# Performance work log

Hardware: AMD Instinct MI355X
Metric: run time of the kernel (lower is better)

## Reference

```python
import jax, jax.numpy as jnp
import numpy as np

HIDDEN = 4096
N_HEADS = 32
HEAD_DIM = HIDDEN // N_HEADS
BATCH = 2
SEQ = 2048
ROPE_BASE = 10000.0


def _rope_cos_sin(seq_len, head_dim, dtype):
    inv_freq = 1.0 / (ROPE_BASE ** (jnp.arange(0, head_dim, 2, dtype=jnp.float32) / head_dim))
    t = jnp.arange(seq_len, dtype=jnp.float32)
    freqs = t[:, None] * inv_freq[None, :]          # (seq, head_dim/2)
    emb = jnp.concatenate([freqs, freqs], axis=-1)  # (seq, head_dim)
    return jnp.cos(emb).astype(dtype), jnp.sin(emb).astype(dtype)


def _rotate_half(x):
    d = x.shape[-1] // 2
    return jnp.concatenate([-x[..., d:], x[..., :d]], axis=-1)


def setup_inputs() -> dict:
    key = jax.random.key(0)
    ks = jax.random.split(key, 5)
    s = 1.0 / np.sqrt(HIDDEN)
    return {
        "hidden_states": jax.random.normal(ks[0], (BATCH, SEQ, HIDDEN), dtype=jnp.float32),
        "Wq": jax.random.normal(ks[1], (HIDDEN, HIDDEN), dtype=jnp.float32) * s,
        "Wk": jax.random.normal(ks[2], (HIDDEN, HIDDEN), dtype=jnp.float32) * s,
        "Wv": jax.random.normal(ks[3], (HIDDEN, HIDDEN), dtype=jnp.float32) * s,
        "Wo": jax.random.normal(ks[4], (HIDDEN, HIDDEN), dtype=jnp.float32) * s,
    }


def reference(hidden_states, Wq, Wk, Wv, Wo):
    b, s, _ = hidden_states.shape
    # nn.Linear: y = x @ W.T
    q = hidden_states @ Wq.T
    k = hidden_states @ Wk.T
    v = hidden_states @ Wv.T
    # (b, s, h, d) -> (b, h, s, d)
    q = q.reshape(b, s, N_HEADS, HEAD_DIM).transpose(0, 2, 1, 3)
    k = k.reshape(b, s, N_HEADS, HEAD_DIM).transpose(0, 2, 1, 3)
    v = v.reshape(b, s, N_HEADS, HEAD_DIM).transpose(0, 2, 1, 3)
    cos, sin = _rope_cos_sin(s, HEAD_DIM, hidden_states.dtype)  # (s, d)
    cos = cos[None, None]  # (1,1,s,d)
    sin = sin[None, None]
    q = q * cos + _rotate_half(q) * sin
    k = k * cos + _rotate_half(k) * sin
    scores = jnp.einsum("bhqd,bhkd->bhqk", q, k) / np.sqrt(HEAD_DIM).astype(np.float32)
    attn = jax.nn.softmax(scores, axis=-1)
    out = jnp.einsum("bhqk,bhkd->bhqd", attn, v)
    out = out.transpose(0, 2, 1, 3).reshape(b, s, HIDDEN)
    return out @ Wo.T
```

## Files before the change

kernel.cpp:

```cpp
#include <hip/hip_runtime.h>
#include <hip/hip_bf16.h>

typedef unsigned int u32;

typedef __attribute__((ext_vector_type(4)))  float f32x4;
typedef __attribute__((ext_vector_type(16))) float f32x16;
typedef __attribute__((ext_vector_type(8)))  short s16x8;
typedef __attribute__((ext_vector_type(4)))  short s16x4;
typedef __attribute__((ext_vector_type(2)))  short s16x2;

#define MFMA16(acc, a, b) asm("v_mfma_f32_16x16x32_bf16 %0, %1, %2, %0" : "+v"(acc) : "v"(a), "v"(b))
#define MFMA32(acc, a, b) asm("v_mfma_f32_32x32x16_bf16 %0, %1, %2, %0" : "+v"(acc) : "v"(a), "v"(b))

__device__ __forceinline__ short f2bf(float f) {
  u32 u = __float_as_uint(f);
  return (short)((u + 0x7fffu + ((u >> 16) & 1u)) >> 16);
}
__device__ __forceinline__ float bf2f(short h) {
  return __uint_as_float(((u32)(unsigned short)h) << 16);
}
__device__ __forceinline__ void gload_lds16(const void* g, void* l) {
  __builtin_amdgcn_global_load_lds((const __attribute__((address_space(1))) u32*)g,
                                   (__attribute__((address_space(3))) u32*)l, 16, 0, 0);
}

__global__ __launch_bounds__(256) void cvt_f32_bf16(const float* __restrict__ in,
                                                    short* __restrict__ out, int n8) {
  int i = blockIdx.x * 256 + threadIdx.x;
  if (i >= n8) return;
  const f32x4* p = (const f32x4*)in;
  f32x4 a = p[2 * i], b = p[2 * i + 1];
  s16x8 o;
#pragma unroll
  for (int j = 0; j < 4; ++j) { o[j] = f2bf(a[j]); o[4 + j] = f2bf(b[j]); }
  *(s16x8*)(out + 8 * (size_t)i) = o;
}

__global__ __launch_bounds__(256) void rope_tables(float* __restrict__ ct, float* __restrict__ st) {
  int tid = blockIdx.x * 256 + threadIdx.x;
  int i = tid & 63, s = tid >> 6;
  float inv = exp2f(-(float)(2 * i) * (13.287712379549449f / 128.0f));
  float ang = (float)s * inv;
  ct[tid] = cosf(ang);
  st[tid] = sinf(ang);
}

__global__ __launch_bounds__(256) void rope_apply(short* __restrict__ x, const float* __restrict__ ct,
                                                  const float* __restrict__ st, float scale) {
  int tid = blockIdx.x * 256 + threadIdx.x;
  int quad = tid & 15;
  int h = (tid >> 4) & 31;
  int s = (tid >> 9) & 2047;
  int b = tid >> 20;
  size_t off = ((size_t)(b * 2048 + s)) * 4096 + h * 128 + quad * 4;
  s16x4 lo = *(s16x4*)(x + off);
  s16x4 hi = *(s16x4*)(x + off + 64);
  f32x4 c = *(const f32x4*)(ct + s * 64 + quad * 4);
  f32x4 sn = *(const f32x4*)(st + s * 64 + quad * 4);
  s16x4 nlo, nhi;
#pragma unroll
  for (int j = 0; j < 4; ++j) {
    float fl = bf2f(lo[j]), fh = bf2f(hi[j]);
    nlo[j] = f2bf((fl * c[j] - fh * sn[j]) * scale);
    nhi[j] = f2bf((fh * c[j] + fl * sn[j]) * scale);
  }
  *(s16x4*)(x + off) = nlo;
  *(s16x4*)(x + off + 64) = nhi;
}

template <int MODE>
__global__ __launch_bounds__(512) void gemm_nt(const short* __restrict__ A, const short* __restrict__ B,
                                               void* __restrict__ Cv, int M, int N, int K) {
  __shared__ short lds[65536];
  const int tid = threadIdx.x, lane = tid & 63, wid = tid >> 6;
  const int nbn = N >> 8;
  const int nwg = (M >> 8) * nbn;
  int bid = blockIdx.x;
  bid = (bid & 7) * (nwg >> 3) + (bid >> 3);
  const int m0 = (bid / nbn) << 8, n0 = (bid % nbn) << 8;
  const int wm = wid >> 2, wn = wid & 3;
  const int l15 = lane & 15, l16 = lane >> 4;
  const int r8 = lane >> 3, c8 = lane & 7;
  const int sw8 = (c8 ^ r8) << 3;

  f32x4 acc[8][4] = {};
  const int nt = K >> 6;

#pragma unroll
  for (int c = 0; c < 4; ++c) {
    const int chunk = wid * 4 + c;
    const int row = chunk * 8 + r8;
    gload_lds16(A + (size_t)(m0 + row) * K + sw8, &lds[chunk * 512]);
    gload_lds16(B + (size_t)(n0 + row) * K + sw8, &lds[32768 + chunk * 512]);
  }
  __syncthreads();

  for (int t = 0; t < nt; ++t) {
    const int bb = (t & 1) << 14;
    const int nb = bb ^ 16384;
    const short* As = &lds[bb];
    const short* Bs = &lds[32768 + bb];
    if (t + 1 < nt) {
      const int kt2 = (t + 1) << 6;
#pragma unroll
      for (int c = 0; c < 4; ++c) {
        const int chunk = wid * 4 + c;
        const int row = chunk * 8 + r8;
        gload_lds16(A + (size_t)(m0 + row) * K + kt2 + sw8, &lds[nb + chunk * 512]);
        gload_lds16(B + (size_t)(n0 + row) * K + kt2 + sw8, &lds[32768 + nb + chunk * 512]);
      }
    }
#pragma unroll
    for (int ph = 0; ph < 4; ++ph) {
      const int mh = ph >> 1, kc = ph & 1;
      s16x8 af[4], bfr[4];
#pragma unroll
      for (int i = 0; i < 4; ++i) {
        const int ra = wm * 128 + mh * 64 + i * 16 + l15;
        const int rb = wn * 64 + i * 16 + l15;
        const int cb = kc * 64 + l16 * 16;
        af[i]  = *(const s16x8*)((const char*)As + ra * 128 + (cb ^ ((ra & 7) << 4)));
        bfr[i] = *(const s16x8*)((const char*)Bs + rb * 128 + (cb ^ ((rb & 7) << 4)));
      }
#pragma unroll
      for (int i = 0; i < 4; ++i)
#pragma unroll
        for (int j = 0; j < 4; ++j) MFMA16(acc[mh * 4 + i][j], af[i], bfr[j]);
    }
    __syncthreads();
  }

  float* Cf = (float*)Cv;
  short* Cs = (short*)Cv;
  const int mrb = m0 + wm * 128 + l16 * 4;
  const int ncb = n0 + wn * 64 + l15;
#pragma unroll
  for (int mi = 0; mi < 8; ++mi)
#pragma unroll
    for (int ni = 0; ni < 4; ++ni)
#pragma unroll
      for (int r = 0; r < 4; ++r) {
        const int mm = mrb + mi * 16 + r;
        const int nn = ncb + ni * 16;
        const float v = acc[mi][ni][r];
        if constexpr (MODE == 0) {
          Cf[(size_t)mm * N + nn] = v;
        } else if constexpr (MODE == 1) {
          Cs[(size_t)mm * N + nn] = f2bf(v);
        } else {
          size_t idx = ((size_t)((mm >> 11) * 32 + (nn >> 7)) * 128 + (nn & 127)) * 2048 + (mm & 2047);
          Cs[idx] = f2bf(v);
        }
      }
}

__global__ __launch_bounds__(256) void attn_fwd(const short* __restrict__ Q, const short* __restrict__ K,
                                                const short* __restrict__ V, short* __restrict__ O) {
  __shared__ short Klds[64 * 136];
  __shared__ short Vt[128 * 72];
  __shared__ short Plds[4 * 32 * 72];
  const int tid = threadIdx.x, lane = tid & 63, wid = tid >> 6;
  const int q31 = lane & 31, hh = lane >> 5;
  int bid = blockIdx.x;
  bid = (bid & 7) * 128 + (bid >> 3);
  const int bh = bid >> 4, qt = bid & 15;
  const int b = bh >> 5, h = bh & 31;
  const size_t base = (size_t)b * 2048 * 4096 + h * 128;
  const short* Vg = V + ((size_t)(b * 32 + h)) * 128 * 2048;
  const int q0 = qt * 128 + wid * 32;

  s16x8 qf[8];
#pragma unroll
  for (int kc = 0; kc < 8; ++kc)
    qf[kc] = *(const s16x8*)(Q + base + (size_t)(q0 + q31) * 4096 + kc * 16 + hh * 8);

  f32x16 o[4] = {};
  float lsum = 0.0f;
  const float L2E = 1.44269504f, BIAS = 14.4269504f;

  for (int kv0 = 0; kv0 < 2048; kv0 += 64) {
    __syncthreads();
#pragma unroll
    for (int j = 0; j < 4; ++j) {
      int ci = tid + j * 256;
      int row = ci >> 4, cc = ci & 15;
      *(s16x8*)(&Klds[row * 136 + cc * 8]) =
          *(const s16x8*)(K + base + (size_t)(kv0 + row) * 4096 + cc * 8);
    }
#pragma unroll
    for (int j = 0; j < 4; ++j) {
      int ci = tid + j * 256;
      int row = ci >> 3, cc = ci & 7;
      *(s16x8*)(&Vt[row * 72 + cc * 8]) =
          *(const s16x8*)(Vg + (size_t)row * 2048 + kv0 + cc * 8);
    }
    __syncthreads();

    f32x16 st[2] = {};
    __builtin_amdgcn_s_setprio(1);
#pragma unroll
    for (int t = 0; t < 2; ++t)
#pragma unroll
      for (int kc = 0; kc < 8; ++kc) {
        s16x8 ak = *(const s16x8*)(&Klds[(t * 32 + q31) * 136 + kc * 16 + hh * 8]);
        MFMA32(st[t], ak, qf[kc]);
      }
    __builtin_amdgcn_s_setprio(0);

    float rs = 0.0f;
#pragma unroll
    for (int t = 0; t < 2; ++t)
#pragma unroll
      for (int r = 0; r < 16; ++r) {
        float p = exp2f(__builtin_fmaf(st[t][r], L2E, -BIAS));
        st[t][r] = p;
        rs += p;
      }
    rs += __shfl_xor(rs, 32);
    lsum += rs;

    short* Pw = &Plds[wid * 2304 + q31 * 72];
#pragma unroll
    for (int t = 0; t < 2; ++t)
#pragma unroll
      for (int rr = 0; rr < 16; rr += 2) {
        int kv = t * 32 + (rr & 3) + 8 * (rr >> 2) + 4 * hh;
        s16x2 pk;
        pk[0] = f2bf(st[t][rr]);
        pk[1] = f2bf(st[t][rr + 1]);
        *(s16x2*)(Pw + kv) = pk;
      }

    __builtin_amdgcn_s_setprio(1);
#pragma unroll
    for (int kc = 0; kc < 4; ++kc) {
      s16x8 bp = *(const s16x8*)(Pw + kc * 16 + hh * 8);
#pragma unroll
      for (int dt = 0; dt < 4; ++dt) {
        s16x8 av = *(const s16x8*)(&Vt[(dt * 32 + q31) * 72 + kc * 16 + hh * 8]);
        MFMA32(o[dt], av, bp);
      }
    }
    __builtin_amdgcn_s_setprio(0);
  }

  const float invl = 1.0f / lsum;
  short* Og = O + base + (size_t)(q0 + q31) * 4096;
#pragma unroll
  for (int dt = 0; dt < 4; ++dt)
#pragma unroll
    for (int g = 0; g < 4; ++g) {
      s16x4 w;
#pragma unroll
      for (int j = 0; j < 4; ++j) w[j] = f2bf(o[dt][g * 4 + j] * invl);
      *(s16x4*)(Og + dt * 32 + g * 8 + 4 * hh) = w;
    }
}

extern "C" void kernel_launch(void* const* d_in, const int* in_sizes, int n_in,
                              void* d_out, int out_size, void* d_ws, size_t ws_size,
                              hipStream_t stream) {
  (void)in_sizes; (void)n_in; (void)out_size;
  const float* X  = (const float*)d_in[0];
  const float* Wq = (const float*)d_in[1];
  const float* Wk = (const float*)d_in[2];
  const float* Wv = (const float*)d_in[3];
  const float* Wo = (const float*)d_in[4];
  float* out = (float*)d_out;

  const size_t SZ = 33554432;
  if (ws_size < 6 * SZ + 2 * 524288) return;
  char* ws = (char*)d_ws;
  short* Xb = (short*)(ws);
  short* Wb = (short*)(ws + SZ);
  short* Qb = (short*)(ws + 2 * SZ);
  short* Kb = (short*)(ws + 3 * SZ);
  short* Vb = (short*)(ws + 4 * SZ);
  short* Ob = (short*)(ws + 5 * SZ);
  float* ct = (float*)(ws + 6 * SZ);
  float* st = ct + 131072;

  const int N8 = 16777216 / 8;

  cvt_f32_bf16<<<8192, 256, 0, stream>>>(X, Xb, N8);
  rope_tables<<<512, 256, 0, stream>>>(ct, st);

  cvt_f32_bf16<<<8192, 256, 0, stream>>>(Wq, Wb, N8);
  gemm_nt<1><<<256, 512, 0, stream>>>(Xb, Wb, Qb, 4096, 4096, 4096);
  rope_apply<<<8192, 256, 0, stream>>>(Qb, ct, st, 0.08838834764831845f);

  cvt_f32_bf16<<<8192, 256, 0, stream>>>(Wk, Wb, N8);
  gemm_nt<1><<<256, 512, 0, stream>>>(Xb, Wb, Kb, 4096, 4096, 4096);
  rope_apply<<<8192, 256, 0, stream>>>(Kb, ct, st, 1.0f);

  cvt_f32_bf16<<<8192, 256, 0, stream>>>(Wv, Wb, N8);
  gemm_nt<2><<<256, 512, 0, stream>>>(Xb, Wb, Vb, 4096, 4096, 4096);

  attn_fwd<<<1024, 256, 0, stream>>>(Qb, Kb, Vb, Ob);

  cvt_f32_bf16<<<8192, 256, 0, stream>>>(Wo, Wb, N8);
  gemm_nt<0><<<256, 512, 0, stream>>>(Ob, Wb, out, 4096, 4096, 4096);
}
```

Measured before the change: 747.1 us.

## Restructure GEMM fragment loads, add occupancy hint, vectorize transposed V store

Sets launch_bounds to ask for 2 workgroups per CU on the GEMM kernel. The inner loop now loads the B fragments for both k-chunks once per tile and reuses them across both m-halves, cutting redundant LDS reads of B. In MODE 2 (the transposed V output), the four consecutive-row results are packed into one 8-byte store instead of four scalar stores. The occupancy hint caps registers per thread, which may spill the 128-float accumulator set, and the LDS footprint of 128KB per block may keep the second workgroup from fitting at all.

```diff
diff --git a/kernel.cpp b/kernel.cpp
--- a/kernel.cpp
+++ b/kernel.cpp
@@ -69,8 +69,8 @@
 }
 
 template <int MODE>
-__global__ __launch_bounds__(512) void gemm_nt(const short* __restrict__ A, const short* __restrict__ B,
-                                               void* __restrict__ Cv, int M, int N, int K) {
+__global__ __launch_bounds__(512, 2) void gemm_nt(const short* __restrict__ A, const short* __restrict__ B,
+                                                  void* __restrict__ Cv, int M, int N, int K) {
   __shared__ short lds[65536];
   const int tid = threadIdx.x, lane = tid & 63, wid = tid >> 6;
   const int nbn = N >> 8;
@@ -110,22 +110,33 @@
         gload_lds16(B + (size_t)(n0 + row) * K + kt2 + sw8, &lds[32768 + nb + chunk * 512]);
       }
     }
-#pragma unroll
-    for (int ph = 0; ph < 4; ++ph) {
-      const int mh = ph >> 1, kc = ph & 1;
-      s16x8 af[4], bfr[4];
-#pragma unroll
-      for (int i = 0; i < 4; ++i) {
-        const int ra = wm * 128 + mh * 64 + i * 16 + l15;
-        const int rb = wn * 64 + i * 16 + l15;
+    s16x8 bf[2][4];
+#pragma unroll
+    for (int kc = 0; kc < 2; ++kc)
+#pragma unroll
+      for (int j = 0; j < 4; ++j) {
+        const int rb = wn * 64 + j * 16 + l15;
         const int cb = kc * 64 + l16 * 16;
-        af[i]  = *(const s16x8*)((const char*)As + ra * 128 + (cb ^ ((ra & 7) << 4)));
-        bfr[i] = *(const s16x8*)((const char*)Bs + rb * 128 + (cb ^ ((rb & 7) << 4)));
-      }
+        bf[kc][j] = *(const s16x8*)((const char*)Bs + rb * 128 + (cb ^ ((rb & 7) << 4)));
+      }
+#pragma unroll
+    for (int mh = 0; mh < 2; ++mh) {
+      s16x8 af[2][4];
+#pragma unroll
+      for (int kc = 0; kc < 2; ++kc)
+#pragma unroll
+        for (int i = 0; i < 4; ++i) {
+          const int ra = wm * 128 + mh * 64 + i * 16 + l15;
+          const int cb = kc * 64 + l16 * 16;
+          af[kc][i] = *(const s16x8*)((const char*)As + ra * 128 + (cb ^ ((ra & 7) << 4)));
+        }
 #pragma unroll
       for (int i = 0; i < 4; ++i)
 #pragma unroll
-        for (int j = 0; j < 4; ++j) MFMA16(acc[mh * 4 + i][j], af[i], bfr[j]);
+        for (int j = 0; j < 4; ++j) {
+          MFMA16(acc[mh * 4 + i][j], af[0][i], bf[0][j]);
+          MFMA16(acc[mh * 4 + i][j], af[1][i], bf[1][j]);
+        }
     }
     __syncthreads();
   }
@@ -137,21 +148,29 @@
 #pragma unroll
   for (int mi = 0; mi < 8; ++mi)
 #pragma unroll
-    for (int ni = 0; ni < 4; ++ni)
-#pragma unroll
-      for (int r = 0; r < 4; ++r) {
-        const int mm = mrb + mi * 16 + r;
+    for (int ni = 0; ni < 4; ++ni) {
+      if constexpr (MODE == 2) {
+        const int mm0 = mrb + mi * 16;
         const int nn = ncb + ni * 16;
-        const float v = acc[mi][ni][r];
-        if constexpr (MODE == 0) {
-          Cf[(size_t)mm * N + nn] = v;
-        } else if constexpr (MODE == 1) {
-          Cs[(size_t)mm * N + nn] = f2bf(v);
-        } else {
-          size_t idx = ((size_t)((mm >> 11) * 32 + (nn >> 7)) * 128 + (nn & 127)) * 2048 + (mm & 2047);
-          Cs[idx] = f2bf(v);
+        size_t idx0 = ((size_t)((mm0 >> 11) * 32 + (nn >> 7)) * 128 + (nn & 127)) * 2048 + (mm0 & 2047);
+        s16x4 w;
+#pragma unroll
+        for (int r = 0; r < 4; ++r) w[r] = f2bf(acc[mi][ni][r]);
+        *(s16x4*)(&Cs[idx0]) = w;
+      } else {
+#pragma unroll
+        for (int r = 0; r < 4; ++r) {
+          const int mm = mrb + mi * 16 + r;
+          const int nn = ncb + ni * 16;
+          const float v = acc[mi][ni][r];
+          if constexpr (MODE == 0) {
+            Cf[(size_t)mm * N + nn] = v;
+          } else {
+            Cs[(size_t)mm * N + nn] = f2bf(v);
+          }
         }
       }
+    }
 }
 
 __global__ __launch_bounds__(256) void attn_fwd(const short* __restrict__ Q, const short* __restrict__ K,
```

New measurement: 738.2 us. Within noise of the previous version (-1.2%).
